# Performance work log

Measured on AMD Instinct MI355X. Metric: run time of the kernel, lower is better.

The kernel has to match this reference:

```python
import jax, jax.numpy as jnp
import numpy as np

EMBED_DIM = 4096
NUM_HEADS = 32
HEAD_DIM = EMBED_DIM // NUM_HEADS  # 128
SEQ_LEN = HEAD_DIM // 2            # 64, forced by the module's RoPE broadcasting
BATCH = 32
W_SCALE = 0.01


def _rope(x, t):
    # Faithful to the original (including its unusual 'bij,d->bidj' axis layout).
    # x: (b, h, s, d); t: (s,)
    d = x.shape[-1]
    inv_freq = 1.0 / (10000.0 ** (jnp.arange(0, d, 2, dtype=jnp.float32) / d))  # (d//2,)
    t3 = t.astype(jnp.float32)[None, None, :]            # (1, 1, s)
    freqs = jnp.einsum('bij,d->bidj', t3, inv_freq)      # (1, 1, d//2, s)
    emb = jnp.concatenate([freqs, freqs], axis=-1)       # (1, 1, d//2, 2s) == (1,1,s,d) since s=d//2
    half = d // 2
    x_rot = jnp.concatenate([-x[..., half:], x[..., :half]], axis=-1)
    return x * jnp.cos(emb) + x_rot * jnp.sin(emb)


def setup_inputs() -> dict:
    key = jax.random.key(0)
    ks = jax.random.split(key, 11)
    e = EMBED_DIM
    def w(k):
        return jax.random.normal(k, (e, e), jnp.float32) * W_SCALE
    def b(k):
        return jax.random.normal(k, (e,), jnp.float32) * W_SCALE
    return {
        'x': jax.random.normal(ks[0], (BATCH, SEQ_LEN, e), jnp.float32),
        't': jnp.arange(SEQ_LEN, dtype=jnp.float32),
        'Wq': w(ks[1]), 'bq': b(ks[2]),
        'Wk': w(ks[3]), 'bk': b(ks[4]),
        'Wv': w(ks[5]), 'bv': b(ks[6]),
        'Wd': w(ks[7]), 'bd': b(ks[8]),
        'Wo': w(ks[9]), 'bo': b(ks[10]),
    }


def reference(x, t, Wq, bq, Wk, bk, Wv, bv, Wd, bd, Wo, bo):
    bsz, s, e = x.shape
    h, d = NUM_HEADS, HEAD_DIM

    def proj(W, bias):
        return (x @ W.T + bias).reshape(bsz, s, h, d).transpose(0, 2, 1, 3)  # (b,h,s,d)

    Q = _rope(proj(Wq, bq), t)
    K = _rope(proj(Wk, bk), t)
    V = proj(Wv, bv)

    gamma = jax.nn.sigmoid(x @ Wd.T + bd).reshape(bsz, s, h, d).transpose(0, 2, 1, 3)
    gc = jnp.cumprod(gamma, axis=2)  # (b,h,s,d), cumprod over sequence
    # mean_d(gc[q,:]/gc[k,:]) == (gc @ (1/gc)^T)/d -- same math as the original's
    # (b,h,q,k,d) D_full.mean(-1), without materializing the rank-5 tensor.
    D_mean = jnp.einsum('bhqd,bhkd->bhqk', gc, 1.0 / gc) / d
    mask = jnp.tril(jnp.ones((s, s), x.dtype))  # causal mask (applied post-mean, same as pre-mean)

    scores = jnp.einsum('bhqd,bhkd->bhqk', Q, K)
    decayed = scores * D_mean * mask
    out = jnp.einsum('bhqk,bhkd->bhqd', decayed, V)  # (b,h,s,d)
    out = out.transpose(0, 2, 1, 3).reshape(bsz, s, e)
    return out @ Wo.T + bo
```

## Files before the change

### kernel.cpp

```cpp
#include <hip/hip_runtime.h>
#include <hip/hip_bf16.h>
#include <cstdint>
#include <cstddef>

typedef __bf16 bf16_t;
typedef __bf16 bf16x4 __attribute__((ext_vector_type(4)));
typedef __bf16 bf16x8 __attribute__((ext_vector_type(8)));
typedef float f32x4 __attribute__((ext_vector_type(4)));

#define D_EMB   4096
#define N_HEADS 32
#define HEAD_D  128
#define SEQ     64
#define NBATCH  32
#define MTOT    2048
#define MB      1048576ULL
#define N4X     2097152
#define N4W     4194304

__global__ __launch_bounds__(256) void cvt_all(
    const float* __restrict__ x,  const float* __restrict__ w0,
    const float* __restrict__ w1, const float* __restrict__ w2,
    const float* __restrict__ w3, const float* __restrict__ w4,
    bf16_t* __restrict__ xb, bf16_t* __restrict__ d0, bf16_t* __restrict__ d1,
    bf16_t* __restrict__ d2, bf16_t* __restrict__ d3, bf16_t* __restrict__ d4) {
  const int i = blockIdx.x * 256 + threadIdx.x;
  const float* s; bf16_t* d; int j;
  if (i < N4X) { s = x; d = xb; j = i; }
  else {
    const int r = i - N4X;
    const int wi = r >> 22;
    j = r & (N4W - 1);
    if (wi == 0)      { s = w0; d = d0; }
    else if (wi == 1) { s = w1; d = d1; }
    else if (wi == 2) { s = w2; d = d2; }
    else if (wi == 3) { s = w3; d = d3; }
    else              { s = w4; d = d4; }
  }
  const float4 v = ((const float4*)s)[j];
  bf16x4 o;
  o[0] = (bf16_t)v.x; o[1] = (bf16_t)v.y; o[2] = (bf16_t)v.z; o[3] = (bf16_t)v.w;
  ((bf16x4*)d)[j] = o;
}

__device__ __forceinline__ void lds_async16(void* lds, const void* gp) {
  __builtin_amdgcn_global_load_lds(
      (const __attribute__((address_space(1))) void*)gp,
      (__attribute__((address_space(3))) void*)lds, 16, 0, 0);
}

__device__ __forceinline__ void gemm_core_bt(const bf16_t* __restrict__ A,
                                             const bf16_t* __restrict__ B,
                                             int K, int m0, int n0,
                                             bf16_t* As, bf16_t* Bs,
                                             f32x4 acc[4][4]) {
  const int tid  = threadIdx.x;
  const int lane = tid & 63;
  const int wave = tid >> 6;
  const int quad = lane >> 4;
  const int l16  = lane & 15;
  const int wm   = (wave >> 1) * 64;
  const int wn   = (wave & 1) * 64;

  const int q0 = tid;
  const int q1 = tid + 256;
  const int r0 = q0 >> 2, c0 = (q0 & 3) * 8;
  const int r1 = q1 >> 2, c1 = (q1 & 3) * 8;

  const bf16_t* Arow0 = A + (size_t)(m0 + r0) * K + c0;
  const bf16_t* Arow1 = A + (size_t)(m0 + r1) * K + c1;
  const bf16_t* Brow0 = B + (size_t)(n0 + r0) * K + c0;
  const bf16_t* Brow1 = B + (size_t)(n0 + r1) * K + c1;

  for (int k0 = 0; k0 < K; k0 += 32) {
    lds_async16(As + q0 * 8, Arow0 + k0);
    lds_async16(As + q1 * 8, Arow1 + k0);
    lds_async16(Bs + q0 * 8, Brow0 + k0);
    lds_async16(Bs + q1 * 8, Brow1 + k0);
    __syncthreads();

    bf16x8 af[4], bfv[4];
#pragma unroll
    for (int i = 0; i < 4; i++)
      af[i] = *(const bf16x8*)&As[(wm + 16 * i + l16) * 32 + quad * 8];
#pragma unroll
    for (int j = 0; j < 4; j++)
      bfv[j] = *(const bf16x8*)&Bs[(wn + 16 * j + l16) * 32 + quad * 8];
#pragma unroll
    for (int i = 0; i < 4; i++)
#pragma unroll
      for (int j = 0; j < 4; j++)
        acc[i][j] = __builtin_amdgcn_mfma_f32_16x16x32_bf16(af[i], bfv[j],
                                                            acc[i][j], 0, 0, 0);
    __syncthreads();
  }
}

__global__ __launch_bounds__(256) void proj_gemm(
    const bf16_t* __restrict__ x,
    const bf16_t* __restrict__ Wq, const float* __restrict__ bq,
    const bf16_t* __restrict__ Wk, const float* __restrict__ bk,
    const bf16_t* __restrict__ Wv, const float* __restrict__ bv,
    const bf16_t* __restrict__ Wd, const float* __restrict__ bd,
    bf16_t* __restrict__ Qp, bf16_t* __restrict__ Kp,
    bf16_t* __restrict__ Vp, bf16_t* __restrict__ Gp) {
  __shared__ __align__(16) bf16_t As[128 * 32];
  __shared__ __align__(16) bf16_t Bs[128 * 32];

  const int m0  = blockIdx.x * 128;
  const int nb  = blockIdx.y;
  const int mat = nb >> 5;
  const int n0  = (nb & 31) * 128;

  const bf16_t* B; const float* bias; bf16_t* dst;
  if (mat == 0)      { B = Wq; bias = bq; dst = Qp; }
  else if (mat == 1) { B = Wk; bias = bk; dst = Kp; }
  else if (mat == 2) { B = Wv; bias = bv; dst = Vp; }
  else               { B = Wd; bias = bd; dst = Gp; }

  f32x4 acc[4][4];
  const f32x4 zero = {0.f, 0.f, 0.f, 0.f};
#pragma unroll
  for (int i = 0; i < 4; i++)
#pragma unroll
    for (int j = 0; j < 4; j++) acc[i][j] = zero;

  gemm_core_bt(x, B, D_EMB, m0, n0, As, Bs, acc);

  const int tid = threadIdx.x, lane = tid & 63, wave = tid >> 6;
  const int quad = lane >> 4, l16 = lane & 15;
  const int wm = (wave >> 1) * 64, wn = (wave & 1) * 64;
  const bool is_g = (mat == 3);

#pragma unroll
  for (int i = 0; i < 4; i++) {
#pragma unroll
    for (int j = 0; j < 4; j++) {
      const int col = n0 + wn + 16 * j + l16;
      const float bv_ = bias[col];
      const int rowb = m0 + wm + 16 * i + quad * 4;
#pragma unroll
      for (int r = 0; r < 4; r++) {
        float v = acc[i][j][r] + bv_;
        if (is_g) v = 1.0f / (1.0f + __expf(-v));
        dst[(size_t)(rowb + r) * D_EMB + col] = (bf16_t)v;
      }
    }
  }
}

__global__ __launch_bounds__(256) void attn_kernel(
    const bf16_t* __restrict__ Qp, const bf16_t* __restrict__ Kp,
    const bf16_t* __restrict__ Vp, const bf16_t* __restrict__ Gp,
    const float* __restrict__ t, bf16_t* __restrict__ attn) {
  __shared__ __align__(16) char smem[65536];
  bf16_t* Qs  = (bf16_t*)smem;
  bf16_t* Ks  = (bf16_t*)(smem + 16384);
  bf16_t* Gs  = (bf16_t*)(smem + 32768);
  bf16_t* IGs = (bf16_t*)(smem + 49152);
  bf16_t* Ps  = (bf16_t*)(smem + 32768);
  bf16_t* Vt  = (bf16_t*)(smem + 32768 + 9216);

  const int tid = threadIdx.x;
  const int lane = tid & 63, wv = tid >> 6;
  const int quad = lane >> 4, l16 = lane & 15;
  const int b = blockIdx.x >> 5, h = blockIdx.x & 31;
  const size_t base = (size_t)(b * SEQ) * D_EMB + (size_t)h * HEAD_D;

  for (int idx = tid; idx < SEQ * HEAD_D; idx += 256) {
    const int s = idx >> 7, d = idx & 127;
    const float invf = __expf(-0.14391156831212787f * (float)s);
    const float theta = t[d & 63] * invf;
    float sn, cs;
    __sincosf(theta, &sn, &cs);
    const size_t po = base + (size_t)s * D_EMB;
    {
      const float v = (float)Qp[po + d];
      const float o = (float)Qp[po + (d ^ 64)];
      const float rot = (d < 64) ? -o : o;
      Qs[idx] = (bf16_t)(v * cs + rot * sn);
    }
    {
      const float v = (float)Kp[po + d];
      const float o = (float)Kp[po + (d ^ 64)];
      const float rot = (d < 64) ? -o : o;
      Ks[idx] = (bf16_t)(v * cs + rot * sn);
    }
  }
  if (tid < HEAD_D) {
    const int d = tid;
    float run = 1.0f;
    for (int s = 0; s < SEQ; s++) {
      run *= (float)Gp[base + (size_t)s * D_EMB + d];
      Gs[s * HEAD_D + d]  = (bf16_t)run;
      IGs[s * HEAD_D + d] = (bf16_t)(1.0f / run);
    }
  }
  __syncthreads();

  f32x4 Sa[4], Da[4];
  const f32x4 zero = {0.f, 0.f, 0.f, 0.f};
#pragma unroll
  for (int j = 0; j < 4; j++) { Sa[j] = zero; Da[j] = zero; }

  for (int k0 = 0; k0 < HEAD_D; k0 += 32) {
    const bf16x8 aq = *(const bf16x8*)&Qs[(wv * 16 + l16) * HEAD_D + quad * 8 + k0];
    const bf16x8 ag = *(const bf16x8*)&Gs[(wv * 16 + l16) * HEAD_D + quad * 8 + k0];
#pragma unroll
    for (int j = 0; j < 4; j++) {
      const bf16x8 bk = *(const bf16x8*)&Ks [(16 * j + l16) * HEAD_D + quad * 8 + k0];
      const bf16x8 bg = *(const bf16x8*)&IGs[(16 * j + l16) * HEAD_D + quad * 8 + k0];
      Sa[j] = __builtin_amdgcn_mfma_f32_16x16x32_bf16(aq, bk, Sa[j], 0, 0, 0);
      Da[j] = __builtin_amdgcn_mfma_f32_16x16x32_bf16(ag, bg, Da[j], 0, 0, 0);
    }
  }
  __syncthreads();

#pragma unroll
  for (int j = 0; j < 4; j++) {
#pragma unroll
    for (int r = 0; r < 4; r++) {
      const int q = wv * 16 + quad * 4 + r;
      const int k = 16 * j + l16;
      const float v = (k <= q) ? Sa[j][r] * Da[j][r] * 0.0078125f : 0.0f;
      Ps[q * 72 + k] = (bf16_t)v;
    }
  }
  for (int idx = tid; idx < SEQ * HEAD_D; idx += 256) {
    const int s = idx >> 7, d = idx & 127;
    Vt[d * 72 + s] = Vp[base + (size_t)s * D_EMB + d];
  }
  __syncthreads();

  f32x4 oa[8];
#pragma unroll
  for (int j = 0; j < 8; j++) oa[j] = zero;
  for (int k0 = 0; k0 < SEQ; k0 += 32) {
    const bf16x8 ap = *(const bf16x8*)&Ps[(wv * 16 + l16) * 72 + quad * 8 + k0];
#pragma unroll
    for (int j = 0; j < 8; j++) {
      const bf16x8 bv = *(const bf16x8*)&Vt[(16 * j + l16) * 72 + quad * 8 + k0];
      oa[j] = __builtin_amdgcn_mfma_f32_16x16x32_bf16(ap, bv, oa[j], 0, 0, 0);
    }
  }
#pragma unroll
  for (int j = 0; j < 8; j++) {
#pragma unroll
    for (int r = 0; r < 4; r++) {
      const int q = wv * 16 + quad * 4 + r;
      attn[(size_t)(b * SEQ + q) * D_EMB + (size_t)h * HEAD_D + 16 * j + l16] =
          (bf16_t)oa[j][r];
    }
  }
}

__global__ __launch_bounds__(256) void out_gemm(
    const bf16_t* __restrict__ A, const bf16_t* __restrict__ Wo,
    const float* __restrict__ bo, float* __restrict__ out) {
  __shared__ __align__(16) bf16_t As[128 * 32];
  __shared__ __align__(16) bf16_t Bs[128 * 32];

  const int m0 = blockIdx.x * 128;
  const int n0 = blockIdx.y * 128;

  f32x4 acc[4][4];
  const f32x4 zero = {0.f, 0.f, 0.f, 0.f};
#pragma unroll
  for (int i = 0; i < 4; i++)
#pragma unroll
    for (int j = 0; j < 4; j++) acc[i][j] = zero;

  gemm_core_bt(A, Wo, D_EMB, m0, n0, As, Bs, acc);

  const int tid = threadIdx.x, lane = tid & 63, wave = tid >> 6;
  const int quad = lane >> 4, l16 = lane & 15;
  const int wm = (wave >> 1) * 64, wn = (wave & 1) * 64;

#pragma unroll
  for (int i = 0; i < 4; i++) {
#pragma unroll
    for (int j = 0; j < 4; j++) {
      const int col = n0 + wn + 16 * j + l16;
      const float bv_ = bo[col];
      const int rowb = m0 + wm + 16 * i + quad * 4;
#pragma unroll
      for (int r = 0; r < 4; r++)
        out[(size_t)(rowb + r) * D_EMB + col] = acc[i][j][r] + bv_;
    }
  }
}

extern "C" void kernel_launch(void* const* d_in, const int* in_sizes, int n_in,
                              void* d_out, int out_size, void* d_ws, size_t ws_size,
                              hipStream_t stream) {
  const float* x  = (const float*)d_in[0];
  const float* t  = (const float*)d_in[1];
  const float* Wq = (const float*)d_in[2];
  const float* bq = (const float*)d_in[3];
  const float* Wk = (const float*)d_in[4];
  const float* bk = (const float*)d_in[5];
  const float* Wv = (const float*)d_in[6];
  const float* bv = (const float*)d_in[7];
  const float* Wd = (const float*)d_in[8];
  const float* bd = (const float*)d_in[9];
  const float* Wo = (const float*)d_in[10];
  const float* bo = (const float*)d_in[11];

  char* ws = (char*)d_ws;
  bf16_t* xb   = (bf16_t*)(ws);
  bf16_t* Wqb  = (bf16_t*)(ws + 16 * MB);
  bf16_t* Wkb  = (bf16_t*)(ws + 48 * MB);
  bf16_t* Wvb  = (bf16_t*)(ws + 80 * MB);
  bf16_t* Wdb  = (bf16_t*)(ws + 112 * MB);
  bf16_t* Wob  = (bf16_t*)(ws + 144 * MB);
  bf16_t* Qp   = (bf16_t*)(ws + 176 * MB);
  bf16_t* Kp   = (bf16_t*)(ws + 192 * MB);
  bf16_t* Vp   = (bf16_t*)(ws + 208 * MB);
  bf16_t* Gp   = (bf16_t*)(ws + 224 * MB);
  bf16_t* attn = (bf16_t*)(ws);

  const int nblk = (N4X + 5 * N4W) / 256;
  cvt_all<<<nblk, 256, 0, stream>>>(x, Wq, Wk, Wv, Wd, Wo,
                                    xb, Wqb, Wkb, Wvb, Wdb, Wob);
  proj_gemm<<<dim3(16, 128), 256, 0, stream>>>(xb, Wqb, bq, Wkb, bk, Wvb, bv,
                                               Wdb, bd, Qp, Kp, Vp, Gp);
  attn_kernel<<<dim3(1024), 256, 0, stream>>>(Qp, Kp, Vp, Gp, t, attn);
  out_gemm<<<dim3(16, 32), 256, 0, stream>>>(attn, Wob, bo, (float*)d_out);
}
```

Measured before the change: 834.9 us.

## Replace projection GEMM with 256x256-tile, 8-wave, pipelined swizzled-LDS kernel

Replaces the 128x128-tile, 256-thread projection GEMM with a 512-thread kernel computing 256x256 tiles over K-steps of 128. It double-buffers A and B in 128KB of LDS using async global-to-LDS loads, XOR-swizzles the LDS layout to avoid bank conflicts, and interleaves staged loads with four MFMA phases using explicit barriers and raised wave priority. Block indices are swizzled so neighbouring blocks share weight tiles. The goal is more arithmetic intensity and better overlap of memory with MFMA in the dominant GEMM. In exchange it adds heavy register pressure and fragile hand-written waitcnt/barrier sequencing.

```diff
diff --git a/kernel.cpp b/kernel.cpp
--- a/kernel.cpp
+++ b/kernel.cpp
@@ -49,6 +49,172 @@
       (__attribute__((address_space(3))) void*)lds, 16, 0, 0);
 }
 
+#define BARRIER() asm volatile("s_barrier" ::: "memory")
+#define WAIT_LGKM0()                                          \
+  do {                                                        \
+    asm volatile("s_waitcnt lgkmcnt(0)" ::: "memory");        \
+    __builtin_amdgcn_sched_barrier(0);                        \
+  } while (0)
+#define WAIT_VM(n) asm volatile("s_waitcnt vmcnt(" #n ")" ::: "memory")
+
+
+#define READ_A(Q)                                                           \
+  do {                                                                      \
+    _Pragma("unroll")                                                       \
+    for (int mi = 0; mi < 2; ++mi) {                                        \
+      _Pragma("unroll")                                                     \
+      for (int ks = 0; ks < 2; ++ks) {                                      \
+        afr[mi][ks] =                                                       \
+            *(const bf16x8*)(As + aoff + ((Q) * 2 + mi) * 1024 + ks * 16384); \
+      }                                                                     \
+    }                                                                       \
+  } while (0)
+
+#define MFMA_PHASE(Q)                                                       \
+  do {                                                                      \
+    __builtin_amdgcn_s_setprio(1);                                          \
+    _Pragma("unroll")                                                       \
+    for (int mi = 0; mi < 2; ++mi) {                                        \
+      _Pragma("unroll")                                                     \
+      for (int j = 0; j < 4; ++j) {                                         \
+        _Pragma("unroll")                                                   \
+        for (int ks = 0; ks < 2; ++ks) {                                    \
+          acc[(Q) * 2 + mi][j] = __builtin_amdgcn_mfma_f32_16x16x32_bf16(   \
+              afr[mi][ks], bfr[j][ks], acc[(Q) * 2 + mi][j], 0, 0, 0);      \
+        }                                                                   \
+      }                                                                     \
+    }                                                                       \
+    __builtin_amdgcn_s_setprio(0);                                          \
+  } while (0)
+
+__global__ __launch_bounds__(512, 2) void proj_gemm8(
+    const bf16_t* __restrict__ x,
+    const bf16_t* __restrict__ Wq, const float* __restrict__ bq,
+    const bf16_t* __restrict__ Wk, const float* __restrict__ bk,
+    const bf16_t* __restrict__ Wv, const float* __restrict__ bv_,
+    const bf16_t* __restrict__ Wd, const float* __restrict__ bd,
+    bf16_t* __restrict__ Qp, bf16_t* __restrict__ Kp,
+    bf16_t* __restrict__ Vp, bf16_t* __restrict__ Gp) {
+  __shared__ __align__(16) char smem[131072];
+
+  const int tid  = threadIdx.x;
+  const int lane = tid & 63;
+  const int wave = tid >> 6;
+  const int quad = lane >> 4, l16 = lane & 15;
+  const int wm = wave >> 2, wn = wave & 3;
+
+  const int bid = (int)blockIdx.x;
+  const int sw  = ((bid & 7) << 6) | (bid >> 3);
+  const int mt  = sw & 7;
+  const int nt  = sw >> 3;
+  const int m0  = mt << 8;
+  const int mat = nt >> 4;
+  const int n0  = (nt & 15) << 8;
+
+  const bf16_t* Bw; const float* bias; bf16_t* dst;
+  if (mat == 0)      { Bw = Wq; bias = bq;  dst = Qp; }
+  else if (mat == 1) { Bw = Wk; bias = bk;  dst = Kp; }
+  else if (mat == 2) { Bw = Wv; bias = bv_; dst = Vp; }
+  else               { Bw = Wd; bias = bd;  dst = Gp; }
+
+  const int p0 = tid * 16, p1 = p0 + 8192;
+  const int o0 = p0 ^ (((p0 >> 7) & 3) << 4);
+  const int o1 = p1 ^ (((p1 >> 7) & 3) << 4);
+  const char* gA0 = (const char*)(x  + (size_t)(m0 + (o0 >> 6)) * D_EMB) + (o0 & 63);
+  const char* gA1 = (const char*)(x  + (size_t)(m0 + (o1 >> 6)) * D_EMB) + (o1 & 63);
+  const char* gB0 = (const char*)(Bw + (size_t)(n0 + (o0 >> 6)) * D_EMB) + (o0 & 63);
+  const char* gB1 = (const char*)(Bw + (size_t)(n0 + (o1 >> 6)) * D_EMB) + (o1 & 63);
+
+  auto stageA = [&](int nb, int ks, int kbyte) {
+    char* d = smem + nb * 65536 + ks * 16384;
+    lds_async16(d + p0, gA0 + kbyte + ks * 64);
+    lds_async16(d + p1, gA1 + kbyte + ks * 64);
+  };
+  auto stageB = [&](int nb, int ks, int kbyte) {
+    char* d = smem + nb * 65536 + 32768 + ks * 16384;
+    lds_async16(d + p0, gB0 + kbyte + ks * 64);
+    lds_async16(d + p1, gB1 + kbyte + ks * 64);
+  };
+
+  const int qsw  = (quad << 4) ^ ((l16 & 6) << 3);
+  const int aoff = (wm * 128 + l16) * 64 + qsw;
+  const int boff = 32768 + (wn * 64 + l16) * 64 + qsw;
+
+  f32x4 acc[8][4];
+  const f32x4 zero = {0.f, 0.f, 0.f, 0.f};
+#pragma unroll
+  for (int i = 0; i < 8; ++i)
+#pragma unroll
+    for (int j = 0; j < 4; ++j) acc[i][j] = zero;
+
+  stageA(0, 0, 0); stageA(0, 1, 0);
+  stageB(0, 0, 0); stageB(0, 1, 0);
+  stageB(1, 0, 128); stageB(1, 1, 128);
+  WAIT_VM(4);
+  BARRIER();
+
+  bf16x8 bfr[4][2], afr[2][2];
+
+#pragma unroll 1
+  for (int T = 0; T < 64; ++T) {
+    const int buf = T & 1;
+    const char* As = smem + buf * 65536;
+    const int kb1 = (T + 1) << 7;
+    const int kb2 = (T + 2) << 7;
+
+#pragma unroll
+    for (int j = 0; j < 4; ++j)
+#pragma unroll
+      for (int ks = 0; ks < 2; ++ks)
+        bfr[j][ks] = *(const bf16x8*)(As + boff + j * 1024 + ks * 16384);
+    READ_A(0);
+    if (T < 63) stageA(buf ^ 1, 0, kb1);
+    BARRIER();
+    WAIT_LGKM0();
+    MFMA_PHASE(0);
+    BARRIER();
+
+    READ_A(1);
+    if (T < 63) stageA(buf ^ 1, 1, kb1);
+    if (T < 62) stageB(buf, 0, kb2);
+    BARRIER();
+    WAIT_LGKM0();
+    MFMA_PHASE(1);
+    BARRIER();
+
+    READ_A(2);
+    if (T < 62) stageB(buf, 1, kb2);
+    BARRIER();
+    WAIT_LGKM0();
+    MFMA_PHASE(2);
+    BARRIER();
+
+    READ_A(3);
+    BARRIER();
+    WAIT_LGKM0();
+    MFMA_PHASE(3);
+    if (T < 62) { WAIT_VM(4); } else { WAIT_VM(0); }
+    BARRIER();
+  }
+
+  const bool is_g = (mat == 3);
+#pragma unroll
+  for (int j = 0; j < 4; ++j) {
+    const int col = n0 + wn * 64 + j * 16 + l16;
+    const float bb = bias[col];
+#pragma unroll
+    for (int mi = 0; mi < 8; ++mi) {
+      const int rowb = m0 + wm * 128 + mi * 16 + quad * 4;
+#pragma unroll
+      for (int r = 0; r < 4; ++r) {
+        float v = acc[mi][j][r] + bb;
+        if (is_g) v = 1.0f / (1.0f + __expf(-v));
+        dst[(size_t)(rowb + r) * D_EMB + col] = (bf16_t)v;
+      }
+    }
+  }
+}
+
 __device__ __forceinline__ void gemm_core_bt(const bf16_t* __restrict__ A,
                                              const bf16_t* __restrict__ B,
                                              int K, int m0, int n0,
@@ -93,59 +259,6 @@
         acc[i][j] = __builtin_amdgcn_mfma_f32_16x16x32_bf16(af[i], bfv[j],
                                                             acc[i][j], 0, 0, 0);
     __syncthreads();
-  }
-}
-
-__global__ __launch_bounds__(256) void proj_gemm(
-    const bf16_t* __restrict__ x,
-    const bf16_t* __restrict__ Wq, const float* __restrict__ bq,
-    const bf16_t* __restrict__ Wk, const float* __restrict__ bk,
-    const bf16_t* __restrict__ Wv, const float* __restrict__ bv,
-    const bf16_t* __restrict__ Wd, const float* __restrict__ bd,
-    bf16_t* __restrict__ Qp, bf16_t* __restrict__ Kp,
-    bf16_t* __restrict__ Vp, bf16_t* __restrict__ Gp) {
-  __shared__ __align__(16) bf16_t As[128 * 32];
-  __shared__ __align__(16) bf16_t Bs[128 * 32];
-
-  const int m0  = blockIdx.x * 128;
-  const int nb  = blockIdx.y;
-  const int mat = nb >> 5;
-  const int n0  = (nb & 31) * 128;
-
-  const bf16_t* B; const float* bias; bf16_t* dst;
-  if (mat == 0)      { B = Wq; bias = bq; dst = Qp; }
-  else if (mat == 1) { B = Wk; bias = bk; dst = Kp; }
-  else if (mat == 2) { B = Wv; bias = bv; dst = Vp; }
-  else               { B = Wd; bias = bd; dst = Gp; }
-
-  f32x4 acc[4][4];
-  const f32x4 zero = {0.f, 0.f, 0.f, 0.f};
-#pragma unroll
-  for (int i = 0; i < 4; i++)
-#pragma unroll
-    for (int j = 0; j < 4; j++) acc[i][j] = zero;
-
-  gemm_core_bt(x, B, D_EMB, m0, n0, As, Bs, acc);
-
-  const int tid = threadIdx.x, lane = tid & 63, wave = tid >> 6;
-  const int quad = lane >> 4, l16 = lane & 15;
-  const int wm = (wave >> 1) * 64, wn = (wave & 1) * 64;
-  const bool is_g = (mat == 3);
-
-#pragma unroll
-  for (int i = 0; i < 4; i++) {
-#pragma unroll
-    for (int j = 0; j < 4; j++) {
-      const int col = n0 + wn + 16 * j + l16;
-      const float bv_ = bias[col];
-      const int rowb = m0 + wm + 16 * i + quad * 4;
-#pragma unroll
-      for (int r = 0; r < 4; r++) {
-        float v = acc[i][j][r] + bv_;
-        if (is_g) v = 1.0f / (1.0f + __expf(-v));
-        dst[(size_t)(rowb + r) * D_EMB + col] = (bf16_t)v;
-      }
-    }
   }
 }
 
@@ -322,8 +435,8 @@
   const int nblk = (N4X + 5 * N4W) / 256;
   cvt_all<<<nblk, 256, 0, stream>>>(x, Wq, Wk, Wv, Wd, Wo,
                                     xb, Wqb, Wkb, Wvb, Wdb, Wob);
-  proj_gemm<<<dim3(16, 128), 256, 0, stream>>>(xb, Wqb, bq, Wkb, bk, Wvb, bv,
-                                               Wdb, bd, Qp, Kp, Vp, Gp);
+  proj_gemm8<<<dim3(512), 512, 0, stream>>>(xb, Wqb, bq, Wkb, bk, Wvb, bv,
+                                            Wdb, bd, Qp, Kp, Vp, Gp);
   attn_kernel<<<dim3(1024), 256, 0, stream>>>(Qp, Kp, Vp, Gp, t, attn);
   out_gemm<<<dim3(16, 32), 256, 0, stream>>>(attn, Wob, bo, (float*)d_out);
 }
```

After: 757.1 us. 1.1x faster.
